# Kernel optimization log

Hardware: AMD Instinct MI355X
Metric: run time of the kernel (lower is better)

## Reference

```python
import jax, jax.numpy as jnp
import numpy as np

EMB, HEADS, T_BLK = 1024, 16, 2048
B, T = 2, 2048
HD = EMB // HEADS


def setup_inputs() -> dict:
    key = jax.random.key(0)
    ks = jax.random.split(key, 9)
    s = 1.0 / np.sqrt(EMB)
    return {
        "x": jax.random.normal(ks[0], (B, T, EMB), jnp.float32),
        "Wq": jax.random.normal(ks[1], (EMB, EMB), jnp.float32) * s,
        "bq": jax.random.normal(ks[2], (EMB,), jnp.float32) * s,
        "Wk": jax.random.normal(ks[3], (EMB, EMB), jnp.float32) * s,
        "bk": jax.random.normal(ks[4], (EMB,), jnp.float32) * s,
        "Wv": jax.random.normal(ks[5], (EMB, EMB), jnp.float32) * s,
        "bv": jax.random.normal(ks[6], (EMB,), jnp.float32) * s,
        "Wo": jax.random.normal(ks[7], (EMB, EMB), jnp.float32) * s,
        "bo": jax.random.normal(ks[8], (EMB,), jnp.float32) * s,
    }


def reference(x, Wq, bq, Wk, bk, Wv, bv, Wo, bo):
    # eval mode: dropout is identity
    Bn, Tn, C = x.shape
    def proj(W, b):
        y = x @ W.T + b                      # [B,T,C]
        return y.reshape(Bn, Tn, HEADS, HD).transpose(0, 2, 1, 3)  # [B,H,T,hd]
    q, k, v = proj(Wq, bq), proj(Wk, bk), proj(Wv, bv)
    scores = jnp.einsum('bhqd,bhkd->bhqk', q, k) * (HD ** -0.5)  # [B,H,T,T]
    causal = jnp.tril(jnp.ones((Tn, Tn), dtype=bool))
    scores = jnp.where(causal, scores, -jnp.inf)
    w = jax.nn.softmax(scores, axis=-1)
    out = jnp.einsum('bhqk,bhkd->bhqd', w, v)                    # [B,H,T,hd]
    out = out.transpose(0, 2, 1, 3).reshape(Bn, Tn, C)
    return out @ Wo.T + bo
```

## Files before the change

### kernel.cpp

```cpp
#include <hip/hip_runtime.h>
#include <stdint.h>

#define EMB   1024
#define HEADS 16
#define HD    64
#define BB    2
#define TT    2048
#define MTOT  (BB*TT)

#define ELX (4194304u)
#define ELW (1048576u)

#define CSCALE (0.125f * 1.44269504088896f)

typedef __attribute__((ext_vector_type(8))) short short8;
typedef __attribute__((ext_vector_type(4))) float f32x4;
typedef __attribute__((ext_vector_type(4))) unsigned short us4;

__device__ __forceinline__ float bf2f(ushort u) {
  union { uint32_t u; float f; } x; x.u = ((uint32_t)u) << 16; return x.f;
}
__device__ __forceinline__ ushort f2bf(float f) {
  union { float f; uint32_t u; } x; x.f = f;
  uint32_t u = x.u;
  u += 0x7fffu + ((u >> 16) & 1u);
  return (ushort)(u >> 16);
}
__device__ __forceinline__ uint32_t pack2(uint32_t lo, uint32_t hi) {
  return (lo >> 16) | (hi & 0xFFFF0000u);
}
__device__ __forceinline__ short8 cvt8_rne(const float* f) {
  f32x4 a = *(const f32x4*)f;
  f32x4 b = *(const f32x4*)(f + 4);
  short8 r;
  r[0] = (short)f2bf(a[0]); r[1] = (short)f2bf(a[1]);
  r[2] = (short)f2bf(a[2]); r[3] = (short)f2bf(a[3]);
  r[4] = (short)f2bf(b[0]); r[5] = (short)f2bf(b[1]);
  r[6] = (short)f2bf(b[2]); r[7] = (short)f2bf(b[3]);
  return r;
}

__device__ __forceinline__ void gll16(const void* g, void* l) {
  __builtin_amdgcn_global_load_lds((const __attribute__((address_space(1))) void*)g,
                                   (__attribute__((address_space(3))) void*)l,
                                   16, 0, 0);
}

__global__ void detect_dtype(const uint32_t* __restrict__ x, int* __restrict__ flag) {
  const int lane = threadIdx.x & 63;
  int cnt = 0;
#pragma unroll
  for (int i = 0; i < 4; ++i) {
    const uint32_t v = x[lane * 4 + i];
    const uint32_t e = ((v & 0xFFFFu) >> 7) & 0xFFu;
    cnt += (e >= 0x70u && e <= 0x8Fu) ? 1 : 0;
  }
#pragma unroll
  for (int off = 1; off < 64; off <<= 1) cnt += __shfl_xor(cnt, off);
  if (lane == 0) *flag = (cnt > 128) ? 1 : 0;
}

__global__ __launch_bounds__(256) void convert4(const void* __restrict__ w0,
                                                const void* __restrict__ w1,
                                                const void* __restrict__ w2,
                                                const void* __restrict__ x,
                                                ushort* __restrict__ w3,
                                                ushort* __restrict__ xb,
                                                const int* __restrict__ flag) {
  const size_t i = ((size_t)blockIdx.x * 256 + threadIdx.x) * 8;
  const int isbf = *flag;
  if (i < 3u * ELW) {
    const int wi = (int)(i >> 20);
    const size_t off = i & (ELW - 1);
    const void* src = (wi == 0) ? w0 : (wi == 1) ? w1 : w2;
    if (isbf) *(short8*)(w3 + i) = *(const short8*)((const ushort*)src + off);
    else      *(short8*)(w3 + i) = cvt8_rne((const float*)src + off);
  } else {
    const size_t j = i - 3u * ELW;
    if (isbf) *(short8*)(xb + j) = *(const short8*)((const ushort*)x + j);
    else      *(short8*)(xb + j) = cvt8_rne((const float*)x + j);
  }
}

__global__ __launch_bounds__(256) void convertW1(const void* __restrict__ wo,
                                                 ushort* __restrict__ dst,
                                                 const int* __restrict__ flag) {
  const size_t i = ((size_t)blockIdx.x * 256 + threadIdx.x) * 8;
  if (*flag) *(short8*)(dst + i) = *(const short8*)((const ushort*)wo + i);
  else       *(short8*)(dst + i) = cvt8_rne((const float*)wo + i);
}

#define ASZ (256 * 64)
#define BSZ (192 * 64)

__device__ __forceinline__ void qkv_core(const ushort* __restrict__ xb,
                                         const ushort* __restrict__ W,
                                         int m0, int n0r,
                                         ushort* As0, ushort* Bs0,
                                         f32x4 acc[8][3]) {
  const int tid  = threadIdx.x;
  const int w    = tid >> 6;
  const int lane = tid & 63;
  const int quad = lane >> 4;
  const int l16  = lane & 15;
  const int wr   = w >> 2, wc = w & 3;

  const int prow = tid >> 3;
  const int c    = tid & 7;
  const int sw   = c ^ (prow & 7);
  const int rsw  = l16 & 7;

  auto stageB = [&](int cur, int kt) {
#pragma unroll
    for (int g = 0; g < 3; ++g)
      gll16(W + (size_t)(n0r + g * 64 + prow) * EMB + kt * 64 + sw * 8,
            Bs0 + cur * BSZ + g * 4096 + w * 512);
  };
  auto stageA = [&](int cur, int kt) {
#pragma unroll
    for (int g = 0; g < 4; ++g)
      gll16(xb + (size_t)(m0 + g * 64 + prow) * EMB + kt * 64 + sw * 8,
            As0 + cur * ASZ + g * 4096 + w * 512);
  };

  stageB(0, 0);
  stageA(0, 0);
  __syncthreads();

  for (int t = 0; t < 16; ++t) {
    const int cur = t & 1, nxt = cur ^ 1;
    if (t < 15) {
      stageB(nxt, t + 1);
      stageA(nxt, t + 1);
    }

    const ushort* Ab = As0 + cur * ASZ;
    const ushort* Bb = Bs0 + cur * BSZ;
    short8 bf_[3][2];
#pragma unroll
    for (int ni = 0; ni < 3; ++ni)
#pragma unroll
      for (int ks = 0; ks < 2; ++ks)
        bf_[ni][ks] = *(const short8*)&Bb[(wc * 48 + ni * 16 + l16) * 64 +
                                          ((ks * 4 + quad) ^ rsw) * 8];
#pragma unroll
    for (int mi = 0; mi < 8; ++mi) {
      const int arow = (wr * 128 + mi * 16 + l16) * 64;
      short8 a0 = *(const short8*)&Ab[arow + ((quad) ^ rsw) * 8];
      short8 a1 = *(const short8*)&Ab[arow + ((4 + quad) ^ rsw) * 8];
#pragma unroll
      for (int ni = 0; ni < 3; ++ni) {
        acc[mi][ni] = __builtin_amdgcn_mfma_f32_16x16x32_bf16(a0, bf_[ni][0], acc[mi][ni], 0, 0, 0);
        acc[mi][ni] = __builtin_amdgcn_mfma_f32_16x16x32_bf16(a1, bf_[ni][1], acc[mi][ni], 0, 0, 0);
      }
    }
    __syncthreads();
  }
}

__global__ __launch_bounds__(512, 2) void qkv_pipe(const ushort* __restrict__ xb,
                                                   const ushort* __restrict__ w3,
                                                   const void* __restrict__ bq,
                                                   const void* __restrict__ bk,
                                                   const void* __restrict__ bv,
                                                   ushort* __restrict__ qo,
                                                   ushort* __restrict__ ko,
                                                   ushort* __restrict__ vo,
                                                   const int* __restrict__ flag) {
  __shared__ __align__(16) ushort As2[2 * ASZ];
  __shared__ __align__(16) ushort Bs2[2 * BSZ];
  const int bid = blockIdx.x;
  const int xcd = bid & 7;
  const int mt  = xcd * 2 + ((bid >> 3) & 1);
  const int nt  = bid >> 4;
  const int m0  = mt * 256;
  const int n0r = nt * 192;

  f32x4 acc[8][3];
#pragma unroll
  for (int a = 0; a < 8; ++a)
#pragma unroll
    for (int b = 0; b < 3; ++b) acc[a][b] = (f32x4){0.f, 0.f, 0.f, 0.f};

  qkv_core(xb, w3, m0, n0r, As2, Bs2, acc);

  const int isbf = *flag;
  const int tid  = threadIdx.x;
  const int w    = tid >> 6;
  const int lane = tid & 63;
  const int quad = lane >> 4;
  const int l16  = lane & 15;
  const int wr   = w >> 2, wc = w & 3;

#pragma unroll
  for (int ni = 0; ni < 3; ++ni) {
    const int n   = n0r + wc * 48 + ni * 16 + l16;
    const int mat = n >> 10, nn = n & 1023;
    const void* bias = (mat == 0) ? bq : (mat == 1) ? bk : bv;
    const float bv_ = isbf ? bf2f(((const ushort*)bias)[nn]) : ((const float*)bias)[nn];
    const int h = nn >> 6, d = nn & 63;
    const float sc = (mat == 0) ? CSCALE : 1.0f;
    ushort* dqk = (mat == 0) ? qo : ko;
#pragma unroll
    for (int mi = 0; mi < 8; ++mi) {
      const int m = m0 + wr * 128 + mi * 16 + quad * 4;
      const int b = m >> 11, tt = m & (TT - 1);
      if (mat == 2) {
        us4 pk;
#pragma unroll
        for (int r = 0; r < 4; ++r) pk[r] = f2bf(acc[mi][ni][r] + bv_);
        *(us4*)&vo[((size_t)((b * HEADS + h) * HD + d)) * TT + tt] = pk;
      } else {
#pragma unroll
        for (int r = 0; r < 4; ++r)
          dqk[((size_t)((b * HEADS + h) * TT + tt + r)) * HD + d] =
              f2bf((acc[mi][ni][r] + bv_) * sc);
      }
    }
  }
}

__global__ __launch_bounds__(256) void attn3(const ushort* __restrict__ qw,
                                             const ushort* __restrict__ kw,
                                             const ushort* __restrict__ vtw,
                                             ushort* __restrict__ out) {
  __shared__ __align__(16) ushort Ks[64 * 64];
  __shared__ __align__(16) ushort Vts[64 * 64];
  __shared__ __align__(16) ushort Ps[4][16 * 64];

  const int bid = blockIdx.x;
  const int j  = bid >> 8;
  const int r8 = bid & 255;
  const int qh = r8 & 31;
  const int bh = j * 8 + (r8 >> 5);
  int qt;
  if      (j == 0) qt = qh;
  else if (j == 1) qt = 31 - qh;
  else if (j == 2) qt = (qh + 16) & 31;
  else             qt = 31 - ((qh + 16) & 31);
  const int h = bh & (HEADS - 1);
  const int b = bh >> 4;

  const int tid  = threadIdx.x;
  const int w    = tid >> 6;
  const int lane = tid & 63;
  const int quad = lane >> 4;
  const int l16  = lane & 15;
  const int rsw  = l16 & 7;

  const size_t hoff = ((size_t)(b * HEADS + h)) * TT * HD;
  const ushort* Qg = qw + hoff;
  const ushort* Kg = kw + hoff;
  const ushort* Vg = vtw + hoff;
  const int q0 = qt * 64;

  short8 qf[2];
  {
    const ushort* qrow = Qg + (size_t)(q0 + w * 16 + l16) * HD;
    qf[0] = *(const short8*)(qrow + quad * 8);
    qf[1] = *(const short8*)(qrow + 32 + quad * 8);
  }

  const int row = tid >> 2;
  const int cq  = (tid & 3) * 2;
  const int s0  = (cq)     ^ (row & 7);
  const int s1  = (cq + 1) ^ (row & 7);
  const int c0  = cq * 8;
  const ushort* Kbase = Kg + (size_t)row * HD + c0;
  const ushort* Vbase = Vg + (size_t)row * TT + c0;

  float lsp[4] = {0.f, 0.f, 0.f, 0.f};
  f32x4 O[4];
#pragma unroll
  for (int ni = 0; ni < 4; ++ni) O[ni] = (f32x4){0.f, 0.f, 0.f, 0.f};

  auto compute_tile = [&](int kt) {
    f32x4 s[4];
#pragma unroll
    for (int ni = 0; ni < 4; ++ni) s[ni] = (f32x4){0.f, 0.f, 0.f, 0.f};
#pragma unroll
    for (int ks = 0; ks < 2; ++ks) {
#pragma unroll
      for (int ni = 0; ni < 4; ++ni) {
        short8 kb = *(const short8*)&Ks[(ni * 16 + l16) * 64 +
                                        ((ks * 4 + quad) ^ rsw) * 8];
        s[ni] = __builtin_amdgcn_mfma_f32_16x16x32_bf16(kb, qf[ks], s[ni], 0, 0, 0);
      }
    }
    if (kt == qt) {
      const int qq = w * 16 + l16;
#pragma unroll
      for (int ni = 0; ni < 4; ++ni) {
#pragma unroll
        for (int r = 0; r < 4; ++r)
          if (ni * 16 + quad * 4 + r > qq) s[ni][r] = -__builtin_inff();
      }
    }
#pragma unroll
    for (int ni = 0; ni < 4; ++ni) {
      union { float f; uint32_t u; } p0, p1, p2, p3;
      p0.f = exp2f(s[ni][0]); p1.f = exp2f(s[ni][1]);
      p2.f = exp2f(s[ni][2]); p3.f = exp2f(s[ni][3]);
      lsp[ni] += (p0.f + p1.f) + (p2.f + p3.f);
      uint2 dw;
      dw.x = pack2(p0.u, p1.u);
      dw.y = pack2(p2.u, p3.u);
      const int slot = (2 * ni + (quad >> 1)) ^ rsw;
      *(uint2*)&Ps[w][l16 * 64 + slot * 8 + (quad & 1) * 4] = dw;
    }
#pragma unroll
    for (int ks = 0; ks < 2; ++ks) {
      short8 a = *(const short8*)&Ps[w][l16 * 64 + ((ks * 4 + quad) ^ rsw) * 8];
#pragma unroll
      for (int ni = 0; ni < 4; ++ni) {
        short8 vb = *(const short8*)&Vts[(ni * 16 + l16) * 64 +
                                         ((ks * 4 + quad) ^ rsw) * 8];
        O[ni] = __builtin_amdgcn_mfma_f32_16x16x32_bf16(a, vb, O[ni], 0, 0, 0);
      }
    }
  };

  short8 ak0, ak1, av0, av1;
  short8 bk0, bk1, bv0, bv1;
  ak0 = *(const short8*)(Kbase);
  ak1 = *(const short8*)(Kbase + 8);
  av0 = *(const short8*)(Vbase);
  av1 = *(const short8*)(Vbase + 8);

  for (int kt = 0; kt <= qt; ) {
    __syncthreads();
    *(short8*)&Ks[row * 64 + s0 * 8]  = ak0;
    *(short8*)&Ks[row * 64 + s1 * 8]  = ak1;
    *(short8*)&Vts[row * 64 + s0 * 8] = av0;
    *(short8*)&Vts[row * 64 + s1 * 8] = av1;
    if (kt + 1 <= qt) {
      const size_t ko_ = (size_t)(kt + 1) * 64 * HD;
      bk0 = *(const short8*)(Kbase + ko_);
      bk1 = *(const short8*)(Kbase + ko_ + 8);
      bv0 = *(const short8*)(Vbase + (kt + 1) * 64);
      bv1 = *(const short8*)(Vbase + (kt + 1) * 64 + 8);
    }
    __syncthreads();
    compute_tile(kt);
    ++kt;
    if (kt > qt) break;

    __syncthreads();
    *(short8*)&Ks[row * 64 + s0 * 8]  = bk0;
    *(short8*)&Ks[row * 64 + s1 * 8]  = bk1;
    *(short8*)&Vts[row * 64 + s0 * 8] = bv0;
    *(short8*)&Vts[row * 64 + s1 * 8] = bv1;
    if (kt + 1 <= qt) {
      const size_t ko_ = (size_t)(kt + 1) * 64 * HD;
      ak0 = *(const short8*)(Kbase + ko_);
      ak1 = *(const short8*)(Kbase + ko_ + 8);
      av0 = *(const short8*)(Vbase + (kt + 1) * 64);
      av1 = *(const short8*)(Vbase + (kt + 1) * 64 + 8);
    }
    __syncthreads();
    compute_tile(kt);
    ++kt;
  }

  float lst = (lsp[0] + lsp[1]) + (lsp[2] + lsp[3]);
  lst += __shfl_xor(lst, 16);
  lst += __shfl_xor(lst, 32);

#pragma unroll
  for (int r = 0; r < 4; ++r) {
    const float inv = 1.0f / __shfl(lst, (lane & 48) | (quad * 4 + r));
    const int t = q0 + w * 16 + quad * 4 + r;
#pragma unroll
    for (int ni = 0; ni < 4; ++ni) {
      out[((size_t)(b * TT + t)) * EMB + h * HD + ni * 16 + l16] = f2bf(O[ni][r] * inv);
    }
  }
}

#define PASZ (128 * 64)

__global__ __launch_bounds__(512, 2) void proj_pipe(const ushort* __restrict__ A,
                                                    const ushort* __restrict__ Wb,
                                                    const void* __restrict__ bo,
                                                    void* __restrict__ out,
                                                    const int* __restrict__ flag) {
  __shared__ __align__(16) ushort As2[2 * PASZ];
  __shared__ __align__(16) ushort Bs2[2 * PASZ];
  const int bid = blockIdx.x;
  const int xcd = bid & 7;
  const int mt  = xcd * 4 + ((bid >> 3) & 3);
  const int nt  = bid >> 5;
  const int m0  = mt * 128;
  const int n0  = nt * 128;

  const int tid  = threadIdx.x;
  const int w    = tid >> 6;
  const int lane = tid & 63;
  const int quad = lane >> 4;
  const int l16  = lane & 15;
  const int wr   = w >> 2, wc = w & 3;

  const int prow = tid >> 3;
  const int sw   = (tid & 7) ^ (prow & 7);
  const int rsw  = l16 & 7;

  f32x4 acc[4][2];
#pragma unroll
  for (int i = 0; i < 4; ++i)
#pragma unroll
    for (int jj = 0; jj < 2; ++jj) acc[i][jj] = (f32x4){0.f, 0.f, 0.f, 0.f};

  auto stageA = [&](int cur, int kt) {
#pragma unroll
    for (int g = 0; g < 2; ++g)
      gll16(A + (size_t)(m0 + g * 64 + prow) * EMB + kt * 64 + sw * 8,
            As2 + cur * PASZ + g * 4096 + w * 512);
  };
  auto stageB = [&](int cur, int kt) {
#pragma unroll
    for (int g = 0; g < 2; ++g)
      gll16(Wb + (size_t)(n0 + g * 64 + prow) * EMB + kt * 64 + sw * 8,
            Bs2 + cur * PASZ + g * 4096 + w * 512);
  };

  stageA(0, 0);
  stageB(0, 0);
  __syncthreads();

  for (int t = 0; t < 16; ++t) {
    const int cur = t & 1, nxt = cur ^ 1;
    if (t < 15) {
      stageA(nxt, t + 1);
      stageB(nxt, t + 1);
    }
    const ushort* Ab = As2 + cur * PASZ;
    const ushort* Bb = Bs2 + cur * PASZ;
    short8 bf_[2][2];
#pragma unroll
    for (int ni = 0; ni < 2; ++ni)
#pragma unroll
      for (int ks = 0; ks < 2; ++ks)
        bf_[ni][ks] = *(const short8*)&Bb[(wc * 32 + ni * 16 + l16) * 64 +
                                          ((ks * 4 + quad) ^ rsw) * 8];
#pragma unroll
    for (int mi = 0; mi < 4; ++mi) {
      const int arow = (wr * 64 + mi * 16 + l16) * 64;
      short8 a0 = *(const short8*)&Ab[arow + ((quad) ^ rsw) * 8];
      short8 a1 = *(const short8*)&Ab[arow + ((4 + quad) ^ rsw) * 8];
#pragma unroll
      for (int ni = 0; ni < 2; ++ni) {
        acc[mi][ni] = __builtin_amdgcn_mfma_f32_16x16x32_bf16(a0, bf_[ni][0], acc[mi][ni], 0, 0, 0);
        acc[mi][ni] = __builtin_amdgcn_mfma_f32_16x16x32_bf16(a1, bf_[ni][1], acc[mi][ni], 0, 0, 0);
      }
    }
    __syncthreads();
  }

  const int isbf = *flag;
#pragma unroll
  for (int ni = 0; ni < 2; ++ni) {
    const int n = n0 + wc * 32 + ni * 16 + l16;
    const float bv_ = isbf ? bf2f(((const ushort*)bo)[n]) : ((const float*)bo)[n];
#pragma unroll
    for (int mi = 0; mi < 4; ++mi) {
#pragma unroll
      for (int r = 0; r < 4; ++r) {
        const int m = m0 + wr * 64 + mi * 16 + quad * 4 + r;
        const float v = acc[mi][ni][r] + bv_;
        if (isbf) ((ushort*)out)[(size_t)m * EMB + n] = f2bf(v);
        else      ((float*) out)[(size_t)m * EMB + n] = v;
      }
    }
  }
}

extern "C" void kernel_launch(void* const* d_in, const int* in_sizes, int n_in,
                              void* d_out, int out_size, void* d_ws, size_t ws_size,
                              hipStream_t stream) {
  const void* x  = d_in[0];
  const void* Wq = d_in[1];
  const void* bq = d_in[2];
  const void* Wk = d_in[3];
  const void* bk = d_in[4];
  const void* Wv = d_in[5];
  const void* bv = d_in[6];
  const void* Wo = d_in[7];
  const void* bo = d_in[8];

  int* flag = (int*)d_ws;
  ushort* base = (ushort*)((char*)d_ws + 256);

  ushort* q_ws  = base;
  ushort* k_ws  = q_ws + ELX;
  ushort* vt_ws = k_ws + ELX;
  ushort* w3    = vt_ws + ELX;
  ushort* o_ws  = vt_ws + ELX;
  ushort* xb    = (ushort*)d_out;
  ushort* wo_b  = q_ws;

  detect_dtype<<<dim3(1), dim3(64), 0, stream>>>((const uint32_t*)x, flag);
  convert4<<<dim3(3584), dim3(256), 0, stream>>>(Wq, Wk, Wv, x, w3, xb, flag);
  qkv_pipe<<<dim3(256), dim3(512), 0, stream>>>(xb, w3, bq, bk, bv,
                                                q_ws, k_ws, vt_ws, flag);
  attn3<<<dim3(1024), dim3(256), 0, stream>>>(q_ws, k_ws, vt_ws, o_ws);
  convertW1<<<dim3(512), dim3(256), 0, stream>>>(Wo, wo_b, flag);
  proj_pipe<<<dim3(256), dim3(512), 0, stream>>>(o_ws, wo_b, bo, d_out, flag);
}
```

Baseline: 198.5 us.

## Fuse dtype probe and Wo conversion into kernels, double-buffer attention K/V tiles

The dtype detection moves into convert4, where every block probes it redundantly, and the separate detect_dtype launch is dropped. The Wo fp32-to-bf16 conversion kernel is removed; proj_pipe now loads fp32 weights into registers, packs them to bf16 by truncation and writes them into LDS inside the pipelined loop. Attention processes two K/V tiles per barrier pair using double-buffered LDS, which halves the number of syncs. Together this removes two launches and one global round trip. The cost is truncation instead of round-to-nearest for Wo, extra register pressure, more LDS in attn3, and redundant probing work in every convert4 block.

New measurement: 199.6 us. No clear change (+0.6%).

```diff
diff --git a/kernel.cpp b/kernel.cpp
--- a/kernel.cpp
+++ b/kernel.cpp
@@ -28,6 +28,16 @@
 }
 __device__ __forceinline__ uint32_t pack2(uint32_t lo, uint32_t hi) {
   return (lo >> 16) | (hi & 0xFFFF0000u);
+}
+__device__ __forceinline__ short8 pack8(f32x4 a, f32x4 b) {
+  union { f32x4 v; uint32_t u[4]; } A, B;
+  A.v = a; B.v = b;
+  union { uint32_t d[4]; short8 s; } R;
+  R.d[0] = pack2(A.u[0], A.u[1]);
+  R.d[1] = pack2(A.u[2], A.u[3]);
+  R.d[2] = pack2(B.u[0], B.u[1]);
+  R.d[3] = pack2(B.u[2], B.u[3]);
+  return R.s;
 }
 __device__ __forceinline__ short8 cvt8_rne(const float* f) {
   f32x4 a = *(const f32x4*)f;
@@ -46,7 +56,7 @@
                                    16, 0, 0);
 }
 
-__global__ void detect_dtype(const uint32_t* __restrict__ x, int* __restrict__ flag) {
+__device__ __forceinline__ int probe_dtype(const uint32_t* __restrict__ x) {
   const int lane = threadIdx.x & 63;
   int cnt = 0;
 #pragma unroll
@@ -57,7 +67,7 @@
   }
 #pragma unroll
   for (int off = 1; off < 64; off <<= 1) cnt += __shfl_xor(cnt, off);
-  if (lane == 0) *flag = (cnt > 128) ? 1 : 0;
+  return (cnt > 128) ? 1 : 0;
 }
 
 __global__ __launch_bounds__(256) void convert4(const void* __restrict__ w0,
@@ -66,9 +76,10 @@
                                                 const void* __restrict__ x,
                                                 ushort* __restrict__ w3,
                                                 ushort* __restrict__ xb,
-                                                const int* __restrict__ flag) {
+                                                int* __restrict__ flag) {
+  const int isbf = probe_dtype((const uint32_t*)x);
+  if (blockIdx.x == 0 && threadIdx.x == 0) *flag = isbf;
   const size_t i = ((size_t)blockIdx.x * 256 + threadIdx.x) * 8;
-  const int isbf = *flag;
   if (i < 3u * ELW) {
     const int wi = (int)(i >> 20);
     const size_t off = i & (ELW - 1);
@@ -80,14 +91,6 @@
     if (isbf) *(short8*)(xb + j) = *(const short8*)((const ushort*)x + j);
     else      *(short8*)(xb + j) = cvt8_rne((const float*)x + j);
   }
-}
-
-__global__ __launch_bounds__(256) void convertW1(const void* __restrict__ wo,
-                                                 ushort* __restrict__ dst,
-                                                 const int* __restrict__ flag) {
-  const size_t i = ((size_t)blockIdx.x * 256 + threadIdx.x) * 8;
-  if (*flag) *(short8*)(dst + i) = *(const short8*)((const ushort*)wo + i);
-  else       *(short8*)(dst + i) = cvt8_rne((const float*)wo + i);
 }
 
 #define ASZ (256 * 64)
@@ -224,8 +227,8 @@
                                              const ushort* __restrict__ kw,
                                              const ushort* __restrict__ vtw,
                                              ushort* __restrict__ out) {
-  __shared__ __align__(16) ushort Ks[64 * 64];
-  __shared__ __align__(16) ushort Vts[64 * 64];
+  __shared__ __align__(16) ushort Ks[2][64 * 64];
+  __shared__ __align__(16) ushort Vts[2][64 * 64];
   __shared__ __align__(16) ushort Ps[4][16 * 64];
 
   const int bid = blockIdx.x;
@@ -274,7 +277,21 @@
 #pragma unroll
   for (int ni = 0; ni < 4; ++ni) O[ni] = (f32x4){0.f, 0.f, 0.f, 0.f};
 
-  auto compute_tile = [&](int kt) {
+  auto loadT = [&](int kt, short8& k0, short8& k1, short8& v0, short8& v1) {
+    const size_t ko_ = (size_t)kt * 64 * HD;
+    k0 = *(const short8*)(Kbase + ko_);
+    k1 = *(const short8*)(Kbase + ko_ + 8);
+    v0 = *(const short8*)(Vbase + kt * 64);
+    v1 = *(const short8*)(Vbase + kt * 64 + 8);
+  };
+  auto writeT = [&](int buf, short8 k0, short8 k1, short8 v0, short8 v1) {
+    *(short8*)&Ks[buf][row * 64 + s0 * 8]  = k0;
+    *(short8*)&Ks[buf][row * 64 + s1 * 8]  = k1;
+    *(short8*)&Vts[buf][row * 64 + s0 * 8] = v0;
+    *(short8*)&Vts[buf][row * 64 + s1 * 8] = v1;
+  };
+
+  auto compute_tile = [&](int kt, int buf) {
     f32x4 s[4];
 #pragma unroll
     for (int ni = 0; ni < 4; ++ni) s[ni] = (f32x4){0.f, 0.f, 0.f, 0.f};
@@ -282,8 +299,8 @@
     for (int ks = 0; ks < 2; ++ks) {
 #pragma unroll
       for (int ni = 0; ni < 4; ++ni) {
-        short8 kb = *(const short8*)&Ks[(ni * 16 + l16) * 64 +
-                                        ((ks * 4 + quad) ^ rsw) * 8];
+        short8 kb = *(const short8*)&Ks[buf][(ni * 16 + l16) * 64 +
+                                            ((ks * 4 + quad) ^ rsw) * 8];
         s[ni] = __builtin_amdgcn_mfma_f32_16x16x32_bf16(kb, qf[ks], s[ni], 0, 0, 0);
       }
     }
@@ -313,53 +330,29 @@
       short8 a = *(const short8*)&Ps[w][l16 * 64 + ((ks * 4 + quad) ^ rsw) * 8];
 #pragma unroll
       for (int ni = 0; ni < 4; ++ni) {
-        short8 vb = *(const short8*)&Vts[(ni * 16 + l16) * 64 +
-                                         ((ks * 4 + quad) ^ rsw) * 8];
+        short8 vb = *(const short8*)&Vts[buf][(ni * 16 + l16) * 64 +
+                                              ((ks * 4 + quad) ^ rsw) * 8];
         O[ni] = __builtin_amdgcn_mfma_f32_16x16x32_bf16(a, vb, O[ni], 0, 0, 0);
       }
     }
   };
 
-  short8 ak0, ak1, av0, av1;
-  short8 bk0, bk1, bv0, bv1;
-  ak0 = *(const short8*)(Kbase);
-  ak1 = *(const short8*)(Kbase + 8);
-  av0 = *(const short8*)(Vbase);
-  av1 = *(const short8*)(Vbase + 8);
-
-  for (int kt = 0; kt <= qt; ) {
+  short8 ek0, ek1, ev0, ev1;
+  short8 ok0, ok1, ov0, ov1;
+  loadT(0, ek0, ek1, ev0, ev1);
+  if (qt >= 1) loadT(1, ok0, ok1, ov0, ov1);
+
+  for (int pt = 0; ; ++pt) {
+    const int t0 = 2 * pt, t1 = t0 + 1;
     __syncthreads();
-    *(short8*)&Ks[row * 64 + s0 * 8]  = ak0;
-    *(short8*)&Ks[row * 64 + s1 * 8]  = ak1;
-    *(short8*)&Vts[row * 64 + s0 * 8] = av0;
-    *(short8*)&Vts[row * 64 + s1 * 8] = av1;
-    if (kt + 1 <= qt) {
-      const size_t ko_ = (size_t)(kt + 1) * 64 * HD;
-      bk0 = *(const short8*)(Kbase + ko_);
-      bk1 = *(const short8*)(Kbase + ko_ + 8);
-      bv0 = *(const short8*)(Vbase + (kt + 1) * 64);
-      bv1 = *(const short8*)(Vbase + (kt + 1) * 64 + 8);
-    }
+    writeT(0, ek0, ek1, ev0, ev1);
+    if (t1 <= qt) writeT(1, ok0, ok1, ov0, ov1);
+    if (t0 + 2 <= qt) loadT(t0 + 2, ek0, ek1, ev0, ev1);
+    if (t1 + 2 <= qt) loadT(t1 + 2, ok0, ok1, ov0, ov1);
     __syncthreads();
-    compute_tile(kt);
-    ++kt;
-    if (kt > qt) break;
-
-    __syncthreads();
-    *(short8*)&Ks[row * 64 + s0 * 8]  = bk0;
-    *(short8*)&Ks[row * 64 + s1 * 8]  = bk1;
-    *(short8*)&Vts[row * 64 + s0 * 8] = bv0;
-    *(short8*)&Vts[row * 64 + s1 * 8] = bv1;
-    if (kt + 1 <= qt) {
-      const size_t ko_ = (size_t)(kt + 1) * 64 * HD;
-      ak0 = *(const short8*)(Kbase + ko_);
-      ak1 = *(const short8*)(Kbase + ko_ + 8);
-      av0 = *(const short8*)(Vbase + (kt + 1) * 64);
-      av1 = *(const short8*)(Vbase + (kt + 1) * 64 + 8);
-    }
-    __syncthreads();
-    compute_tile(kt);
-    ++kt;
+    compute_tile(t0, 0);
+    if (t1 <= qt) compute_tile(t1, 1);
+    if (t1 >= qt) break;
   }
 
   float lst = (lsp[0] + lsp[1]) + (lsp[2] + lsp[3]);
@@ -379,8 +372,93 @@
 
 #define PASZ (128 * 64)
 
+template<bool WBF>
+__device__ __forceinline__ void proj_core(const ushort* __restrict__ A,
+                                          const void* __restrict__ Wo,
+                                          int m0, int n0,
+                                          ushort* As2, ushort* Bs2,
+                                          f32x4 acc[4][2]) {
+  const int tid  = threadIdx.x;
+  const int w    = tid >> 6;
+  const int lane = tid & 63;
+  const int quad = lane >> 4;
+  const int l16  = lane & 15;
+  const int wr   = w >> 2, wc = w & 3;
+
+  const int prow = tid >> 3;
+  const int sw   = (tid & 7) ^ (prow & 7);
+  const int rsw  = l16 & 7;
+
+  const ushort* Wu = (const ushort*)Wo;
+  const float*  Wf = (const float*)Wo;
+  f32x4 wreg[4];
+
+  auto stageA = [&](int cur, int kt) {
+#pragma unroll
+    for (int g = 0; g < 2; ++g)
+      gll16(A + (size_t)(m0 + g * 64 + prow) * EMB + kt * 64 + sw * 8,
+            As2 + cur * PASZ + g * 4096 + w * 512);
+  };
+  auto stageB_gll = [&](int cur, int kt) {
+#pragma unroll
+    for (int g = 0; g < 2; ++g)
+      gll16(Wu + (size_t)(n0 + g * 64 + prow) * EMB + kt * 64 + sw * 8,
+            Bs2 + cur * PASZ + g * 4096 + w * 512);
+  };
+  auto stageB_issue = [&](int kt) {
+#pragma unroll
+    for (int g = 0; g < 2; ++g) {
+      const float* src = Wf + (size_t)(n0 + g * 64 + prow) * EMB + kt * 64 + sw * 8;
+      wreg[2 * g]     = *(const f32x4*)(src);
+      wreg[2 * g + 1] = *(const f32x4*)(src + 4);
+    }
+  };
+  auto stageB_write = [&](int cur) {
+#pragma unroll
+    for (int g = 0; g < 2; ++g)
+      *(short8*)&Bs2[cur * PASZ + ((size_t)g * 512 + tid) * 8] =
+          pack8(wreg[2 * g], wreg[2 * g + 1]);
+  };
+
+  stageA(0, 0);
+  if constexpr (WBF) stageB_gll(0, 0);
+  else { stageB_issue(0); stageB_write(0); }
+  __syncthreads();
+
+  for (int t = 0; t < 16; ++t) {
+    const int cur = t & 1, nxt = cur ^ 1;
+    if (t < 15) {
+      stageA(nxt, t + 1);
+      if constexpr (WBF) stageB_gll(nxt, t + 1);
+      else stageB_issue(t + 1);
+    }
+    const ushort* Ab = As2 + cur * PASZ;
+    const ushort* Bb = Bs2 + cur * PASZ;
+    short8 bf_[2][2];
+#pragma unroll
+    for (int ni = 0; ni < 2; ++ni)
+#pragma unroll
+      for (int ks = 0; ks < 2; ++ks)
+        bf_[ni][ks] = *(const short8*)&Bb[(wc * 32 + ni * 16 + l16) * 64 +
+                                          ((ks * 4 + quad) ^ rsw) * 8];
+#pragma unroll
+    for (int mi = 0; mi < 4; ++mi) {
+      const int arow = (wr * 64 + mi * 16 + l16) * 64;
+      short8 a0 = *(const short8*)&Ab[arow + ((quad) ^ rsw) * 8];
+      short8 a1 = *(const short8*)&Ab[arow + ((4 + quad) ^ rsw) * 8];
+#pragma unroll
+      for (int ni = 0; ni < 2; ++ni) {
+        acc[mi][ni] = __builtin_amdgcn_mfma_f32_16x16x32_bf16(a0, bf_[ni][0], acc[mi][ni], 0, 0, 0);
+        acc[mi][ni] = __builtin_amdgcn_mfma_f32_16x16x32_bf16(a1, bf_[ni][1], acc[mi][ni], 0, 0, 0);
+      }
+    }
+    if (t < 15) { if constexpr (!WBF) stageB_write(nxt); }
+    __syncthreads();
+  }
+}
+
 __global__ __launch_bounds__(512, 2) void proj_pipe(const ushort* __restrict__ A,
-                                                    const ushort* __restrict__ Wb,
+                                                    const void* __restrict__ Wo,
                                                     const void* __restrict__ bo,
                                                     void* __restrict__ out,
                                                     const int* __restrict__ flag) {
@@ -393,6 +471,16 @@
   const int m0  = mt * 128;
   const int n0  = nt * 128;
 
+  f32x4 acc[4][2];
+#pragma unroll
+  for (int i = 0; i < 4; ++i)
+#pragma unroll
+    for (int jj = 0; jj < 2; ++jj) acc[i][jj] = (f32x4){0.f, 0.f, 0.f, 0.f};
+
+  const int isbf = *flag;
+  if (isbf) proj_core<true >(A, Wo, m0, n0, As2, Bs2, acc);
+  else      proj_core<false>(A, Wo, m0, n0, As2, Bs2, acc);
+
   const int tid  = threadIdx.x;
   const int w    = tid >> 6;
   const int lane = tid & 63;
@@ -400,63 +488,6 @@
   const int l16  = lane & 15;
   const int wr   = w >> 2, wc = w & 3;
 
-  const int prow = tid >> 3;
-  const int sw   = (tid & 7) ^ (prow & 7);
-  const int rsw  = l16 & 7;
-
-  f32x4 acc[4][2];
-#pragma unroll
-  for (int i = 0; i < 4; ++i)
-#pragma unroll
-    for (int jj = 0; jj < 2; ++jj) acc[i][jj] = (f32x4){0.f, 0.f, 0.f, 0.f};
-
-  auto stageA = [&](int cur, int kt) {
-#pragma unroll
-    for (int g = 0; g < 2; ++g)
-      gll16(A + (size_t)(m0 + g * 64 + prow) * EMB + kt * 64 + sw * 8,
-            As2 + cur * PASZ + g * 4096 + w * 512);
-  };
-  auto stageB = [&](int cur, int kt) {
-#pragma unroll
-    for (int g = 0; g < 2; ++g)
-      gll16(Wb + (size_t)(n0 + g * 64 + prow) * EMB + kt * 64 + sw * 8,
-            Bs2 + cur * PASZ + g * 4096 + w * 512);
-  };
-
-  stageA(0, 0);
-  stageB(0, 0);
-  __syncthreads();
-
-  for (int t = 0; t < 16; ++t) {
-    const int cur = t & 1, nxt = cur ^ 1;
-    if (t < 15) {
-      stageA(nxt, t + 1);
-      stageB(nxt, t + 1);
-    }
-    const ushort* Ab = As2 + cur * PASZ;
-    const ushort* Bb = Bs2 + cur * PASZ;
-    short8 bf_[2][2];
-#pragma unroll
-    for (int ni = 0; ni < 2; ++ni)
-#pragma unroll
-      for (int ks = 0; ks < 2; ++ks)
-        bf_[ni][ks] = *(const short8*)&Bb[(wc * 32 + ni * 16 + l16) * 64 +
-                                          ((ks * 4 + quad) ^ rsw) * 8];
-#pragma unroll
-    for (int mi = 0; mi < 4; ++mi) {
-      const int arow = (wr * 64 + mi * 16 + l16) * 64;
-      short8 a0 = *(const short8*)&Ab[arow + ((quad) ^ rsw) * 8];
-      short8 a1 = *(const short8*)&Ab[arow + ((4 + quad) ^ rsw) * 8];
-#pragma unroll
-      for (int ni = 0; ni < 2; ++ni) {
-        acc[mi][ni] = __builtin_amdgcn_mfma_f32_16x16x32_bf16(a0, bf_[ni][0], acc[mi][ni], 0, 0, 0);
-        acc[mi][ni] = __builtin_amdgcn_mfma_f32_16x16x32_bf16(a1, bf_[ni][1], acc[mi][ni], 0, 0, 0);
-      }
-    }
-    __syncthreads();
-  }
-
-  const int isbf = *flag;
 #pragma unroll
   for (int ni = 0; ni < 2; ++ni) {
     const int n = n0 + wc * 32 + ni * 16 + l16;
@@ -496,13 +527,10 @@
   ushort* w3    = vt_ws + ELX;
   ushort* o_ws  = vt_ws + ELX;
   ushort* xb    = (ushort*)d_out;
-  ushort* wo_b  = q_ws;
-
-  detect_dtype<<<dim3(1), dim3(64), 0, stream>>>((const uint32_t*)x, flag);
+
   convert4<<<dim3(3584), dim3(256), 0, stream>>>(Wq, Wk, Wv, x, w3, xb, flag);
   qkv_pipe<<<dim3(256), dim3(512), 0, stream>>>(xb, w3, bq, bk, bv,
                                                 q_ws, k_ws, vt_ws, flag);
   attn3<<<dim3(1024), dim3(256), 0, stream>>>(q_ws, k_ws, vt_ws, o_ws);
-  convertW1<<<dim3(512), dim3(256), 0, stream>>>(Wo, wo_b, flag);
-  proj_pipe<<<dim3(256), dim3(512), 0, stream>>>(o_ws, wo_b, bo, d_out, flag);
-}
+  proj_pipe<<<dim3(256), dim3(512), 0, stream>>>(o_ws, Wo, bo, d_out, flag);
+}
```
